# Performance work log

Hardware: AMD Instinct MI355X
Metric: run time of the kernel (lower is better)

The kernel has to match this reference:

```python
import jax, jax.numpy as jnp
import numpy as np
import math

H = 1024
N = 64
DT_MIN, DT_MAX = 1e-3, 1e-1
L_SEQ = 4096


def setup_inputs() -> dict:
    key = jax.random.key(0)
    k1, k2, k3 = jax.random.split(key, 3)
    # C ~ complex normal, stored as (..., 2) real view like torch.view_as_real
    C = jax.random.normal(k1, (H, N // 2, 2), dtype=jnp.float32)
    # log_dt ~ U[log(dt_min), log(dt_max)]
    log_dt = jax.random.uniform(k2, (H,), dtype=jnp.float32) * (
        math.log(DT_MAX) - math.log(DT_MIN)
    ) + math.log(DT_MIN)
    # log_A_real = log(0.5), A_imag = pi * arange(N/2) repeated over H
    log_A_real = jnp.full((H, N // 2), math.log(0.5), dtype=jnp.float32)
    A_imag = math.pi * jnp.broadcast_to(
        jnp.arange(N // 2, dtype=jnp.float32), (H, N // 2)
    )
    return {"C": C, "log_dt": log_dt, "log_A_real": log_A_real, "A_imag": A_imag, "L": L_SEQ}


def reference(C, log_dt, log_A_real, A_imag, L):
    dt = jnp.exp(log_dt)                                  # (H,)
    Cc = jax.lax.complex(C[..., 0], C[..., 1])            # (H, N/2) complex
    A = -jnp.exp(log_A_real) + 1j * A_imag                # (H, N/2) complex
    dtA = A * dt[:, None]                                 # (H, N/2)
    # Vandermonde: exp(dtA * l) for l in [0, L)
    K = dtA[:, :, None] * jnp.arange(L, dtype=jnp.float32)  # (H, N/2, L)
    Cm = Cc * (jnp.exp(dtA) - 1.0) / A                    # (H, N/2)
    K = 2.0 * jnp.einsum("hn,hnl->hl", Cm, jnp.exp(K)).real  # (H, L)
    return K
```

## Files before the change

### kernel.cpp

```cpp
#include <hip/hip_runtime.h>
#include <hip/hip_bf16.h>
#include <math.h>


#define H_DIM 1024
#define NH 32
#define L_DIM 4096
#define TPB 256
#define PER 16

__global__ __launch_bounds__(TPB) void s4d_kernel(
    const float* __restrict__ C,
    const float* __restrict__ log_dt,
    const float* __restrict__ log_A_real,
    const float* __restrict__ A_imag,
    float* __restrict__ out)
{
    const int h = blockIdx.x;
    const int t = threadIdx.x;

    __shared__ float s_w[NH][2];
    __shared__ float s_cm[NH][2];
    __shared__ float s_ta[NH][16][2];
    __shared__ float s_tb[NH][16][2];

    const double TWO_PI  = 6.283185307179586476925286766559;
    const double INV_2PI = 0.15915494309189533576888376337251;

    if (t < NH) {
        const int n = t;
        const float dtf = expf(log_dt[h]);
        const float arf = -expf(log_A_real[h * NH + n]);
        const float aif = A_imag[h * NH + n];
        const float are = arf * dtf;

        double th = (double)aif * (double)dtf;
        th -= floor(th * INV_2PI) * TWO_PI;

        const float mw = expf(are);
        float sn, cs;
        sincosf((float)th, &sn, &cs);
        const float wr = mw * cs;
        const float wi = mw * sn;
        s_w[n][0] = wr;
        s_w[n][1] = wi;

        {
            const float er = wr - 1.0f;
            const float ei = wi;
            const float cr = C[(h * NH + n) * 2 + 0];
            const float ci = C[(h * NH + n) * 2 + 1];
            const float tr = cr * er - ci * ei;
            const float ti = cr * ei + ci * er;
            const float inv = 2.0f / (arf * arf + aif * aif);
            s_cm[n][0] = (tr * arf + ti * aif) * inv;
            s_cm[n][1] = (ti * arf - tr * aif) * inv;
        }

        float ar = wr, ai = wi;
#pragma unroll
        for (int k = 0; k < 4; ++k) {
            const float nr = ar * ar - ai * ai;
            const float ni = 2.0f * ar * ai;
            ar = nr; ai = ni;
        }
        {
            float pr = 1.0f, pi = 0.0f;
#pragma unroll
            for (int j = 0; j < 16; ++j) {
                s_ta[n][j][0] = pr;
                s_ta[n][j][1] = pi;
                const float nr = pr * ar - pi * ai;
                const float ni = pr * ai + pi * ar;
                pr = nr; pi = ni;
            }
        }
        {
            const float m256 = expf(are * 256.0f);
            double p = th * 256.0;
            p -= floor(p * INV_2PI) * TWO_PI;
            float s2, c2;
            sincosf((float)p, &s2, &c2);
            const float br = m256 * c2;
            const float bi = m256 * s2;
            float pr = 1.0f, pi = 0.0f;
#pragma unroll
            for (int j = 0; j < 16; ++j) {
                s_tb[n][j][0] = pr;
                s_tb[n][j][1] = pi;
                const float nr = pr * br - pi * bi;
                const float ni = pr * bi + pi * br;
                pr = nr; pi = ni;
            }
        }
    }
    __syncthreads();

    float acc[PER];
#pragma unroll
    for (int j = 0; j < PER; ++j) acc[j] = 0.0f;

    const int ta_idx = t & 15;
    const int tb_idx = t >> 4;

    for (int n = 0; n < NH; ++n) {
        const float wr = s_w[n][0];
        const float wi = s_w[n][1];
        const float cr = s_cm[n][0];
        const float ci = s_cm[n][1];
        const float tar = s_ta[n][ta_idx][0];
        const float tai = s_ta[n][ta_idx][1];
        const float tbr = s_tb[n][tb_idx][0];
        const float tbi = s_tb[n][tb_idx][1];

        const float pr = tar * tbr - tai * tbi;
        const float pi = tar * tbi + tai * tbr;
        float zr = cr * pr - ci * pi;
        float zi = cr * pi + ci * pr;

#pragma unroll
        for (int j = 0; j < PER; ++j) {
            acc[j] += zr;
            const float nzr = zr * wr - zi * wi;
            const float nzi = zr * wi + zi * wr;
            zr = nzr;
            zi = nzi;
        }
    }

    float4* op = (float4*)(out + (size_t)h * L_DIM + (size_t)t * PER);
#pragma unroll
    for (int j = 0; j < PER / 4; ++j) {
        op[j] = make_float4(acc[4 * j], acc[4 * j + 1], acc[4 * j + 2], acc[4 * j + 3]);
    }
}

extern "C" void kernel_launch(void* const* d_in, const int* in_sizes, int n_in,
                              void* d_out, int out_size, void* d_ws, size_t ws_size,
                              hipStream_t stream) {
    const float* C          = (const float*)d_in[0];
    const float* log_dt     = (const float*)d_in[1];
    const float* log_A_real = (const float*)d_in[2];
    const float* A_imag     = (const float*)d_in[3];
    float* out = (float*)d_out;

    s4d_kernel<<<dim3(H_DIM), dim3(TPB), 0, stream>>>(C, log_dt, log_A_real, A_imag, out);
}
```

Before: 90.13 us.

## Use real second-order recurrence and parallel direct table setup with packed LDS

The inner complex recurrence is replaced by a real two-term recurrence (x_{k+1} = 2Re(w) x_k - |w|^2 x_{k-1}), which cuts the per-step arithmetic roughly in half. The twiddle tables are now computed directly by all 256 threads using exp and hardware sin/cos of reduced angles, instead of serially by 32 threads. Per-mode data is packed into one padded LDS row so the reads become vector loads. The second-order recurrence can amplify rounding error, and fast intrinsics lower precision.

```diff
diff --git a/kernel.cpp b/kernel.cpp
--- a/kernel.cpp
+++ b/kernel.cpp
@@ -8,6 +8,7 @@
 #define L_DIM 4096
 #define TPB 256
 #define PER 16
+#define STRIDE_F 72
 
 __global__ __launch_bounds__(TPB) void s4d_kernel(
     const float* __restrict__ C,
@@ -19,79 +20,63 @@
     const int h = blockIdx.x;
     const int t = threadIdx.x;
 
-    __shared__ float s_w[NH][2];
-    __shared__ float s_cm[NH][2];
-    __shared__ float s_ta[NH][16][2];
-    __shared__ float s_tb[NH][16][2];
+    __shared__ float lds[NH * STRIDE_F];
 
-    const double TWO_PI  = 6.283185307179586476925286766559;
     const double INV_2PI = 0.15915494309189533576888376337251;
 
-    if (t < NH) {
-        const int n = t;
-        const float dtf = expf(log_dt[h]);
-        const float arf = -expf(log_A_real[h * NH + n]);
+    {
+        const int n = t & 31;
+        const int s = t >> 5;
+        const float dtf = __expf(log_dt[h]);
+        const float arf = -__expf(log_A_real[h * NH + n]);
         const float aif = A_imag[h * NH + n];
         const float are = arf * dtf;
+        const double th_rev = (double)aif * (double)dtf * INV_2PI;
 
-        double th = (double)aif * (double)dtf;
-        th -= floor(th * INV_2PI) * TWO_PI;
+        float* base = &lds[n * STRIDE_F];
 
-        const float mw = expf(are);
-        float sn, cs;
-        sincosf((float)th, &sn, &cs);
-        const float wr = mw * cs;
-        const float wi = mw * sn;
-        s_w[n][0] = wr;
-        s_w[n][1] = wi;
+#pragma unroll
+        for (int e = 0; e < 2; ++e) {
+            const int j = 2 * s + e;
+            {
+                const int l = 16 * j;
+                const float mag = __expf(are * (float)l);
+                double u = (double)l * th_rev;
+                u -= floor(u);
+                const float uf = (float)u;
+                base[8 + 2 * j]     = mag * __builtin_amdgcn_cosf(uf);
+                base[8 + 2 * j + 1] = mag * __builtin_amdgcn_sinf(uf);
+            }
+            {
+                const int l = 256 * j;
+                const float mag = __expf(are * (float)l);
+                double u = (double)l * th_rev;
+                u -= floor(u);
+                const float uf = (float)u;
+                base[40 + 2 * j]     = mag * __builtin_amdgcn_cosf(uf);
+                base[40 + 2 * j + 1] = mag * __builtin_amdgcn_sinf(uf);
+            }
+        }
 
-        {
+        if (s == 0) {
+            const float mag = __expf(are);
+            double u = th_rev - floor(th_rev);
+            const float uf = (float)u;
+            const float wr = mag * __builtin_amdgcn_cosf(uf);
+            const float wi = mag * __builtin_amdgcn_sinf(uf);
+            const float cr = C[(h * NH + n) * 2 + 0];
+            const float ci = C[(h * NH + n) * 2 + 1];
             const float er = wr - 1.0f;
             const float ei = wi;
-            const float cr = C[(h * NH + n) * 2 + 0];
-            const float ci = C[(h * NH + n) * 2 + 1];
             const float tr = cr * er - ci * ei;
             const float ti = cr * ei + ci * er;
             const float inv = 2.0f / (arf * arf + aif * aif);
-            s_cm[n][0] = (tr * arf + ti * aif) * inv;
-            s_cm[n][1] = (ti * arf - tr * aif) * inv;
-        }
-
-        float ar = wr, ai = wi;
-#pragma unroll
-        for (int k = 0; k < 4; ++k) {
-            const float nr = ar * ar - ai * ai;
-            const float ni = 2.0f * ar * ai;
-            ar = nr; ai = ni;
-        }
-        {
-            float pr = 1.0f, pi = 0.0f;
-#pragma unroll
-            for (int j = 0; j < 16; ++j) {
-                s_ta[n][j][0] = pr;
-                s_ta[n][j][1] = pi;
-                const float nr = pr * ar - pi * ai;
-                const float ni = pr * ai + pi * ar;
-                pr = nr; pi = ni;
-            }
-        }
-        {
-            const float m256 = expf(are * 256.0f);
-            double p = th * 256.0;
-            p -= floor(p * INV_2PI) * TWO_PI;
-            float s2, c2;
-            sincosf((float)p, &s2, &c2);
-            const float br = m256 * c2;
-            const float bi = m256 * s2;
-            float pr = 1.0f, pi = 0.0f;
-#pragma unroll
-            for (int j = 0; j < 16; ++j) {
-                s_tb[n][j][0] = pr;
-                s_tb[n][j][1] = pi;
-                const float nr = pr * br - pi * bi;
-                const float ni = pr * bi + pi * br;
-                pr = nr; pi = ni;
-            }
+            base[0] = wr;
+            base[1] = wi;
+            base[2] = (tr * arf + ti * aif) * inv;
+            base[3] = (ti * arf - tr * aif) * inv;
+            base[4] = wr + wr;
+            base[5] = -(wr * wr + wi * wi);
         }
     }
     __syncthreads();
@@ -100,31 +85,34 @@
 #pragma unroll
     for (int j = 0; j < PER; ++j) acc[j] = 0.0f;
 
-    const int ta_idx = t & 15;
-    const int tb_idx = t >> 4;
+    const int ta_i = t & 15;
+    const int tb_i = t >> 4;
 
+#pragma unroll 2
     for (int n = 0; n < NH; ++n) {
-        const float wr = s_w[n][0];
-        const float wi = s_w[n][1];
-        const float cr = s_cm[n][0];
-        const float ci = s_cm[n][1];
-        const float tar = s_ta[n][ta_idx][0];
-        const float tai = s_ta[n][ta_idx][1];
-        const float tbr = s_tb[n][tb_idx][0];
-        const float tbi = s_tb[n][tb_idx][1];
+        const float* base = &lds[n * STRIDE_F];
+        const float4 hdr = *(const float4*)base;
+        const float2 pq  = *(const float2*)(base + 4);
+        const float2 ta  = *(const float2*)(base + 8 + 2 * ta_i);
+        const float2 tb  = *(const float2*)(base + 40 + 2 * tb_i);
 
-        const float pr = tar * tbr - tai * tbi;
-        const float pi = tar * tbi + tai * tbr;
-        float zr = cr * pr - ci * pi;
-        float zi = cr * pi + ci * pr;
+        const float pr = ta.x * tb.x - ta.y * tb.y;
+        const float pi = ta.x * tb.y + ta.y * tb.x;
+        const float zr = hdr.z * pr - hdr.w * pi;
+        const float zi = hdr.z * pi + hdr.w * pr;
 
+        float x0 = zr;
+        float x1 = zr * hdr.x - zi * hdr.y;
+        acc[0] += x0;
+        acc[1] += x1;
+        float tq = pq.y * x0;
 #pragma unroll
-        for (int j = 0; j < PER; ++j) {
-            acc[j] += zr;
-            const float nzr = zr * wr - zi * wi;
-            const float nzi = zr * wi + zi * wr;
-            zr = nzr;
-            zi = nzi;
+        for (int j = 2; j < PER; ++j) {
+            const float x2 = fmaf(pq.x, x1, tq);
+            tq = pq.y * x1;
+            acc[j] += x2;
+            x0 = x1;
+            x1 = x2;
         }
     }
 
```

Result: faster. 79.16 us (-12.2%).
